# Kernel optimization log

Hardware: AMD Instinct MI355X
Metric: run time of the kernel (lower is better)

The kernel has to match this reference:

```python
import jax, jax.numpy as jnp
import numpy as np

H, W = 8, 64
HK, WK = 7, 11
N = H * W            # 512 tokens
C = 512              # embed_dim
HEADS = 8
HD = C // HEADS      # 64
SCALE = HD ** -0.5
B = 32


def build_local_mask():
    # Faithful port of the build() mask construction.
    m = np.ones([N, H + HK - 1, W + WK - 1], dtype=np.int32)
    for h in range(H):
        for w in range(W):
            m[h * W + w, h:h + HK, w:w + WK] = 0
    m = m[:, HK // 2:H + HK // 2, WK // 2:W + WK // 2].reshape(-1, N).astype(bool)
    mask = np.where(m, -1e30, 0.0).astype(np.float32)
    return jnp.asarray(mask.reshape(1, 1, N, N))


def setup_inputs() -> dict:
    key = jax.random.key(0)
    k1, k2, k3, k4 = jax.random.split(key, 4)
    return {
        "x": jax.random.normal(k1, (B, N, C), dtype=jnp.float32),
        "w_qkv": jax.random.normal(k2, (C, 3 * C), dtype=jnp.float32) * (C ** -0.5),
        "w_proj": jax.random.normal(k3, (C, C), dtype=jnp.float32) * (C ** -0.5),
        "b_proj": jax.random.normal(k4, (C,), dtype=jnp.float32) * 0.01,
        "mask": build_local_mask(),
    }


def reference(x, w_qkv, w_proj, b_proj, mask):
    b = x.shape[0]
    qkv = x @ w_qkv                                   # [B, N, 3C]
    qkv = qkv.reshape(b, N, 3, HEADS, HD)
    qkv = jnp.transpose(qkv, (2, 0, 3, 1, 4))          # [3, B, heads, N, hd]
    q, k, v = qkv[0], qkv[1], qkv[2]
    attn = jnp.einsum("bhnd,bhmd->bhnm", q * SCALE, k) + mask  # [B, heads, N, N]
    attn = jax.nn.softmax(attn, axis=-1)
    out = jnp.einsum("bhnm,bhmd->bhnd", attn, v)       # [B, heads, N, hd]
    out = jnp.transpose(out, (0, 2, 1, 3)).reshape(b, N, C)
    return out @ w_proj + b_proj
```

## Files before the change

kernel.cpp:

```cpp
#include <hip/hip_runtime.h>
#include <hip/hip_bf16.h>

typedef __attribute__((ext_vector_type(8))) __bf16 bf16x8;
typedef __attribute__((ext_vector_type(4))) float f32x4;

__device__ __forceinline__ unsigned short f2bf(float f) {
    unsigned int u = __float_as_uint(f);
    unsigned int r = u + 0x7FFFu + ((u >> 16) & 1u);
    return (unsigned short)(r >> 16);
}

__device__ __forceinline__ void async_copy16(const unsigned short* g, unsigned short* l) {
    __builtin_amdgcn_global_load_lds(
        (__attribute__((address_space(1))) void*)(g),
        (__attribute__((address_space(3))) void*)(l), 16, 0, 0);
}

__global__ __launch_bounds__(256) void cvt_f32_bf16(const float4* __restrict__ in,
                                                    uint4* __restrict__ out, int n8) {
    int i = blockIdx.x * blockDim.x + threadIdx.x;
    if (i >= n8) return;
    float4 a = in[2 * i], b = in[2 * i + 1];
    union { unsigned short s[8]; uint4 v; } r;
    r.s[0] = f2bf(a.x); r.s[1] = f2bf(a.y); r.s[2] = f2bf(a.z); r.s[3] = f2bf(a.w);
    r.s[4] = f2bf(b.x); r.s[5] = f2bf(b.y); r.s[6] = f2bf(b.z); r.s[7] = f2bf(b.w);
    out[i] = r.v;
}

__global__ __launch_bounds__(256) void transpose_cvt(const float* __restrict__ in,
                                                     unsigned short* __restrict__ out,
                                                     int R, int C) {
    __shared__ float tile[32][33];
    int c0 = blockIdx.x * 32, r0 = blockIdx.y * 32;
    int tx = threadIdx.x, ty = threadIdx.y;
    #pragma unroll
    for (int i = 0; i < 32; i += 8)
        tile[ty + i][tx] = in[(size_t)(r0 + ty + i) * C + c0 + tx];
    __syncthreads();
    #pragma unroll
    for (int i = 0; i < 32; i += 8)
        out[(size_t)(c0 + ty + i) * R + r0 + tx] = f2bf(tile[tx][ty + i]);
}

__device__ __forceinline__ void gemm_core_128(const unsigned short* __restrict__ A,
                                              const unsigned short* __restrict__ Bt,
                                              int K, int m0, int n0, f32x4 acc[4][4]) {
    __shared__ unsigned short As[128 * 64];
    __shared__ unsigned short Bs[128 * 64];
    const int lane = threadIdx.x & 63;
    const int wv   = threadIdx.x >> 6;
    const int wm = (wv >> 1) * 64, wn = (wv & 1) * 64;
    const int l15 = lane & 15, l16 = lane >> 4;

    f32x4 zz = {0.f, 0.f, 0.f, 0.f};
    #pragma unroll
    for (int i = 0; i < 4; ++i)
        #pragma unroll
        for (int j = 0; j < 4; ++j) acc[i][j] = zz;

    for (int k0 = 0; k0 < K; k0 += 64) {
        if (k0) __syncthreads();
        #pragma unroll
        for (int c = 0; c < 4; ++c) {
            int flat16 = c * 256 + (int)threadIdx.x;
            int r  = flat16 >> 3;
            int kk = (flat16 & 7) * 8;
            async_copy16(A  + (size_t)(m0 + r) * K + k0 + kk, As + flat16 * 8);
            async_copy16(Bt + (size_t)(n0 + r) * K + k0 + kk, Bs + flat16 * 8);
        }
        __syncthreads();
        #pragma unroll
        for (int kk = 0; kk < 64; kk += 32) {
            bf16x8 a[4], b[4];
            #pragma unroll
            for (int i = 0; i < 4; ++i)
                a[i] = *(const bf16x8*)(const void*)(As + (wm + i * 16 + l15) * 64 + kk + l16 * 8);
            #pragma unroll
            for (int i = 0; i < 4; ++i)
                b[i] = *(const bf16x8*)(const void*)(Bs + (wn + i * 16 + l15) * 64 + kk + l16 * 8);
            #pragma unroll
            for (int i = 0; i < 4; ++i)
                #pragma unroll
                for (int j = 0; j < 4; ++j)
                    acc[i][j] = __builtin_amdgcn_mfma_f32_16x16x32_bf16(a[i], b[j], acc[i][j], 0, 0, 0);
        }
    }
}

__global__ __launch_bounds__(512, 2) void gemm_qkv_bm(const unsigned short* __restrict__ xb,
                                                      const unsigned short* __restrict__ wT,
                                                      unsigned short* __restrict__ Qb,
                                                      unsigned short* __restrict__ Kb,
                                                      unsigned short* __restrict__ Vb) {
    constexpr int K = 512;
    __shared__ unsigned short As[256 * 64];
    __shared__ unsigned short Bs[128 * 64];

    const int tid  = threadIdx.x;
    const int lane = tid & 63;
    const int wv   = tid >> 6;
    const int wr = wv >> 1, wc = wv & 1;
    const int l15 = lane & 15, l16 = lane >> 4;

    const int bid = blockIdx.x;
    const int xcd = bid & 7, idx = bid >> 3;
    const int mt  = xcd * 8 + idx / 12;
    const int nt  = idx % 12;
    const int m0 = mt * 256, n0 = nt * 128;

    f32x4 acc[4][4];
    f32x4 zz = {0.f, 0.f, 0.f, 0.f};
    #pragma unroll
    for (int i = 0; i < 4; ++i)
        #pragma unroll
        for (int j = 0; j < 4; ++j) acc[i][j] = zz;

    const int r_st  = tid >> 3;
    const int kk_st = (tid & 7) * 8;
    const unsigned short* Arow = xb + (size_t)(m0 + r_st) * K + kk_st;
    const unsigned short* Brow = wT + (size_t)(n0 + r_st) * K + kk_st;

    for (int k0 = 0; k0 < K; k0 += 64) {
        if (k0) __syncthreads();
        #pragma unroll
        for (int c = 0; c < 4; ++c) {
            int flat16 = c * 512 + tid;
            async_copy16(Arow + (size_t)c * 64 * K + k0, As + flat16 * 8);
        }
        #pragma unroll
        for (int c = 0; c < 2; ++c) {
            int flat16 = c * 512 + tid;
            async_copy16(Brow + (size_t)c * 64 * K + k0, Bs + flat16 * 8);
        }
        __syncthreads();
        #pragma unroll
        for (int kk = 0; kk < 64; kk += 32) {
            bf16x8 a[4], b[4];
            #pragma unroll
            for (int i = 0; i < 4; ++i)
                a[i] = *(const bf16x8*)(const void*)(As + (wr * 64 + i * 16 + l15) * 64 + kk + l16 * 8);
            #pragma unroll
            for (int j = 0; j < 4; ++j)
                b[j] = *(const bf16x8*)(const void*)(Bs + (wc * 64 + j * 16 + l15) * 64 + kk + l16 * 8);
            #pragma unroll
            for (int i = 0; i < 4; ++i)
                #pragma unroll
                for (int j = 0; j < 4; ++j)
                    acc[i][j] = __builtin_amdgcn_mfma_f32_16x16x32_bf16(a[i], b[j], acc[i][j], 0, 0, 0);
        }
    }

    #pragma unroll
    for (int j = 0; j < 4; ++j) {
        int col = n0 + wc * 64 + j * 16 + l15;
        int t = col >> 9;
        int within = col & 511;
        int h = within >> 6, d = within & 63;
        unsigned short* dst = (t == 0) ? Qb : (t == 1) ? Kb : Vb;
        float scl = (t == 0) ? 0.125f : 1.0f;
        #pragma unroll
        for (int i = 0; i < 4; ++i)
            #pragma unroll
            for (int e = 0; e < 4; ++e) {
                int row = m0 + wr * 64 + i * 16 + (l16 << 2) + e;
                int bb = row >> 9, n = row & 511;
                dst[(((size_t)bb * 8 + h) * 512 + n) * 64 + d] = f2bf(acc[i][j][e] * scl);
            }
    }
}

__global__ __launch_bounds__(256, 4) void attn_kernel(const unsigned short* __restrict__ Qb,
                                                      const unsigned short* __restrict__ Kb,
                                                      const unsigned short* __restrict__ Vb,
                                                      unsigned short* __restrict__ Ob) {
    __shared__ unsigned short Ks[64 * 72];
    __shared__ unsigned short Vt[64 * 72];
    __shared__ unsigned short Ps[4 * 32 * 72];

    const int bh = blockIdx.x >> 2;
    const int qt = blockIdx.x & 3;
    const int tid = threadIdx.x;
    const int lane = tid & 63;
    const int wv = tid >> 6;
    const int l15 = lane & 15, l16 = lane >> 4;
    const int b = bh >> 3, h = bh & 7;

    const unsigned short* Qp = Qb + (size_t)bh * 512 * 64;
    const unsigned short* Kp = Kb + (size_t)bh * 512 * 64;
    const unsigned short* Vp = Vb + (size_t)bh * 512 * 64;
    unsigned short* Pw = Ps + wv * 32 * 72;

    const int qrow0 = qt * 128 + wv * 32;
    const int qh = qrow0 >> 6;
    const int wq0 = qrow0 & 63;
    const int dead_g = wq0 ? 0 : 3;

    unsigned int wbits = 0;
    {
        int qw[2] = { wq0 + l15, wq0 + 16 + l15 };
        #pragma unroll
        for (int qf = 0; qf < 2; ++qf)
            #pragma unroll
            for (int g = 0; g < 4; ++g)
                #pragma unroll
                for (int j = 0; j < 4; ++j) {
                    int kw = g * 16 + (l16 << 2) + j;
                    int dw = qw[qf] - kw; dw = dw < 0 ? -dw : dw;
                    wbits |= (dw <= 5 ? 1u : 0u) << (qf * 16 + g * 4 + j);
                }
    }

    bf16x8 bQ[2][2];
    #pragma unroll
    for (int qf = 0; qf < 2; ++qf)
        #pragma unroll
        for (int kf = 0; kf < 2; ++kf)
            bQ[qf][kf] = *(const bf16x8*)(const void*)(Qp + (size_t)(qrow0 + qf * 16 + l15) * 64 + kf * 32 + l16 * 8);

    f32x4 o[2][4];
    f32x4 zz = {0.f, 0.f, 0.f, 0.f};
    float mrow[2] = {-INFINITY, -INFINITY}, lrow[2] = {0.f, 0.f};
    #pragma unroll
    for (int qf = 0; qf < 2; ++qf)
        #pragma unroll
        for (int df = 0; df < 4; ++df) o[qf][df] = zz;

    for (int kh = 0; kh < 8; ++kh) {
        int dlo = kh - 2 * qt;
        if (dlo < -3 || dlo > 4) continue;
        __syncthreads();
        #pragma unroll
        for (int c = 0; c < 2; ++c) {
            int flat16 = c * 256 + tid;
            int key = flat16 >> 3, dk = (flat16 & 7) * 8;
            *(uint4*)(void*)(Ks + key * 72 + dk) = *(const uint4*)(const void*)(Kp + ((size_t)(kh * 64 + key) * 64 + dk));
        }
        #pragma unroll
        for (int c = 0; c < 2; ++c) {
            int flat16 = c * 256 + tid;
            int key = flat16 & 63, d8 = flat16 >> 6;
            union { uint4 v; unsigned short s[8]; } t;
            t.v = *(const uint4*)(const void*)(Vp + ((size_t)(kh * 64 + key) * 64 + d8 * 8));
            #pragma unroll
            for (int e = 0; e < 8; ++e) Vt[(d8 * 8 + e) * 72 + key] = t.s[e];
        }
        __syncthreads();

        int adq = qh - kh; adq = adq < 0 ? -adq : adq;
        if (adq > 3) continue;

        f32x4 s[2][4];
        #pragma unroll
        for (int qf = 0; qf < 2; ++qf)
            #pragma unroll
            for (int g = 0; g < 4; ++g) s[qf][g] = zz;
        #pragma unroll
        for (int g = 0; g < 4; ++g) {
            if (g == dead_g) continue;
            bf16x8 aK0 = *(const bf16x8*)(const void*)(Ks + (g * 16 + l15) * 72 + 0  + l16 * 8);
            bf16x8 aK1 = *(const bf16x8*)(const void*)(Ks + (g * 16 + l15) * 72 + 32 + l16 * 8);
            #pragma unroll
            for (int qf = 0; qf < 2; ++qf) {
                s[qf][g] = __builtin_amdgcn_mfma_f32_16x16x32_bf16(aK0, bQ[qf][0], s[qf][g], 0, 0, 0);
                s[qf][g] = __builtin_amdgcn_mfma_f32_16x16x32_bf16(aK1, bQ[qf][1], s[qf][g], 0, 0, 0);
            }
        }

        float tmax[2] = {-1e30f, -1e30f};
        #pragma unroll
        for (int qf = 0; qf < 2; ++qf) {
            #pragma unroll
            for (int g = 0; g < 4; ++g) {
                if (g == dead_g) continue;
                #pragma unroll
                for (int j = 0; j < 4; ++j) {
                    float v = ((wbits >> (qf * 16 + g * 4 + j)) & 1u) ? s[qf][g][j] : -1e30f;
                    s[qf][g][j] = v;
                    tmax[qf] = fmaxf(tmax[qf], v);
                }
            }
            float t = tmax[qf];
            t = fmaxf(t, __shfl_xor(t, 16));
            t = fmaxf(t, __shfl_xor(t, 32));
            tmax[qf] = t;
        }

        #pragma unroll
        for (int qf = 0; qf < 2; ++qf) {
            float mnew = fmaxf(mrow[qf], tmax[qf]);
            float fs = __expf(mrow[qf] - mnew);
            mrow[qf] = mnew;
            lrow[qf] *= fs;
            #pragma unroll
            for (int j = 0; j < 4; ++j) {
                float fso = __shfl(fs, (l16 << 2) + j);
                #pragma unroll
                for (int df = 0; df < 4; ++df) o[qf][df][j] *= fso;
            }
        }

        #pragma unroll
        for (int qf = 0; qf < 2; ++qf) {
            float lsum = 0.f;
            #pragma unroll
            for (int g = 0; g < 4; ++g) {
                unsigned int lo, hi;
                if (g == dead_g) {
                    lo = 0u; hi = 0u;
                } else {
                    float e0 = __expf(s[qf][g][0] - mrow[qf]);
                    float e1 = __expf(s[qf][g][1] - mrow[qf]);
                    float e2 = __expf(s[qf][g][2] - mrow[qf]);
                    float e3 = __expf(s[qf][g][3] - mrow[qf]);
                    lsum += (e0 + e1) + (e2 + e3);
                    asm("v_cvt_pk_bf16_f32 %0, %1, %2" : "=v"(lo) : "v"(e0), "v"(e1));
                    asm("v_cvt_pk_bf16_f32 %0, %1, %2" : "=v"(hi) : "v"(e2), "v"(e3));
                }
                uint2 w; w.x = lo; w.y = hi;
                *(uint2*)(void*)(Pw + (qf * 16 + l15) * 72 + g * 16 + (l16 << 2)) = w;
            }
            float t = lsum;
            t += __shfl_xor(t, 16);
            t += __shfl_xor(t, 32);
            lrow[qf] += t;
        }
        asm volatile("" ::: "memory");

        #pragma unroll
        for (int kf = 0; kf < 2; ++kf) {
            bf16x8 aP0 = *(const bf16x8*)(const void*)(Pw + (0 * 16 + l15) * 72 + kf * 32 + l16 * 8);
            bf16x8 aP1 = *(const bf16x8*)(const void*)(Pw + (1 * 16 + l15) * 72 + kf * 32 + l16 * 8);
            #pragma unroll
            for (int df = 0; df < 4; ++df) {
                bf16x8 bV = *(const bf16x8*)(const void*)(Vt + (df * 16 + l15) * 72 + kf * 32 + l16 * 8);
                o[0][df] = __builtin_amdgcn_mfma_f32_16x16x32_bf16(aP0, bV, o[0][df], 0, 0, 0);
                o[1][df] = __builtin_amdgcn_mfma_f32_16x16x32_bf16(aP1, bV, o[1][df], 0, 0, 0);
            }
        }
    }

    #pragma unroll
    for (int qf = 0; qf < 2; ++qf) {
        float linv = 1.0f / lrow[qf];
        #pragma unroll
        for (int j = 0; j < 4; ++j) {
            float lj = __shfl(linv, (l16 << 2) + j);
            int q = qrow0 + qf * 16 + (l16 << 2) + j;
            size_t base = ((size_t)b * 512 + q) * 512 + h * 64;
            #pragma unroll
            for (int df = 0; df < 4; ++df)
                Ob[base + df * 16 + l15] = f2bf(o[qf][df][j] * lj);
        }
    }
}

__global__ __launch_bounds__(256) void gemm_proj(const unsigned short* __restrict__ Ab,
                                                 const unsigned short* __restrict__ wT,
                                                 const float* __restrict__ bias,
                                                 float* __restrict__ out) {
    f32x4 acc[4][4];
    int m0 = blockIdx.y * 128, n0 = blockIdx.x * 128;
    gemm_core_128(Ab, wT, 512, m0, n0, acc);
    const int lane = threadIdx.x & 63, wv = threadIdx.x >> 6;
    const int wm = (wv >> 1) * 64, wn = (wv & 1) * 64;
    const int l15 = lane & 15, l16 = lane >> 4;
    #pragma unroll
    for (int j = 0; j < 4; ++j) {
        int col = n0 + wn + j * 16 + l15;
        float bb = bias[col];
        #pragma unroll
        for (int i = 0; i < 4; ++i)
            #pragma unroll
            for (int e = 0; e < 4; ++e) {
                int row = m0 + wm + i * 16 + (l16 << 2) + e;
                out[(size_t)row * 512 + col] = acc[i][j][e] + bb;
            }
    }
}

extern "C" void kernel_launch(void* const* d_in, const int* in_sizes, int n_in,
                              void* d_out, int out_size, void* d_ws, size_t ws_size,
                              hipStream_t stream) {
    const float* x      = (const float*)d_in[0];
    const float* w_qkv  = (const float*)d_in[1];
    const float* w_proj = (const float*)d_in[2];
    const float* b_proj = (const float*)d_in[3];
    float* out = (float*)d_out;

    char* ws = (char*)d_ws;
    unsigned short* xb     = (unsigned short*)(ws);
    unsigned short* wqkvT  = (unsigned short*)(ws + 16777216);
    unsigned short* wprojT = (unsigned short*)(ws + 18350080);
    unsigned short* Qb     = (unsigned short*)(ws + 18874368);
    unsigned short* Kb     = (unsigned short*)(ws + 35651584);
    unsigned short* Vb     = (unsigned short*)(ws + 52428800);
    unsigned short* Ob     = xb;

    cvt_f32_bf16<<<4096, 256, 0, stream>>>((const float4*)x, (uint4*)xb, 1048576);
    transpose_cvt<<<dim3(48, 16), dim3(32, 8), 0, stream>>>(w_qkv, wqkvT, 512, 1536);
    transpose_cvt<<<dim3(16, 16), dim3(32, 8), 0, stream>>>(w_proj, wprojT, 512, 512);
    gemm_qkv_bm<<<768, 512, 0, stream>>>(xb, wqkvT, Qb, Kb, Vb);
    attn_kernel<<<1024, 256, 0, stream>>>(Qb, Kb, Vb, Ob);
    gemm_proj<<<dim3(4, 128), 256, 0, stream>>>(Ob, wprojT, b_proj, out);
}
```

Measured before the change: 120.5 us.

## Fuse x fp32-to-bf16 conversion into QKV GEMM A-tile loads

Removes the separate cvt_f32_bf16 pass over x and has the QKV GEMM stage fp32 x tiles into LDS, converting them to bf16 at fragment-load time with packed cvt instructions. This drops one full read and write of x through memory and one kernel launch. In exchange the A tile uses twice the LDS bytes and the block tiling drops from 256x128 with 512 threads and XCD-aware ordering to 128x128 with 256 threads on a plain 2D grid. It also adds conversion ALU work inside the GEMM inner loop and re-reads fp32 x once per N tile.

```diff
diff --git a/kernel.cpp b/kernel.cpp
--- a/kernel.cpp
+++ b/kernel.cpp
@@ -16,15 +16,21 @@
         (__attribute__((address_space(3))) void*)(l), 16, 0, 0);
 }
 
-__global__ __launch_bounds__(256) void cvt_f32_bf16(const float4* __restrict__ in,
-                                                    uint4* __restrict__ out, int n8) {
-    int i = blockIdx.x * blockDim.x + threadIdx.x;
-    if (i >= n8) return;
-    float4 a = in[2 * i], b = in[2 * i + 1];
-    union { unsigned short s[8]; uint4 v; } r;
-    r.s[0] = f2bf(a.x); r.s[1] = f2bf(a.y); r.s[2] = f2bf(a.z); r.s[3] = f2bf(a.w);
-    r.s[4] = f2bf(b.x); r.s[5] = f2bf(b.y); r.s[6] = f2bf(b.z); r.s[7] = f2bf(b.w);
-    out[i] = r.v;
+__device__ __forceinline__ void async_copy16f(const float* g, float* l) {
+    __builtin_amdgcn_global_load_lds(
+        (__attribute__((address_space(1))) void*)(g),
+        (__attribute__((address_space(3))) void*)(l), 16, 0, 0);
+}
+
+__device__ __forceinline__ bf16x8 cvt8(const float* p) {
+    f32x4 lo = *(const f32x4*)(const void*)p;
+    f32x4 hi = *(const f32x4*)(const void*)(p + 4);
+    union { unsigned int u[4]; bf16x8 v; } r;
+    asm("v_cvt_pk_bf16_f32 %0, %1, %2" : "=v"(r.u[0]) : "v"(lo[0]), "v"(lo[1]));
+    asm("v_cvt_pk_bf16_f32 %0, %1, %2" : "=v"(r.u[1]) : "v"(lo[2]), "v"(lo[3]));
+    asm("v_cvt_pk_bf16_f32 %0, %1, %2" : "=v"(r.u[2]) : "v"(hi[0]), "v"(hi[1]));
+    asm("v_cvt_pk_bf16_f32 %0, %1, %2" : "=v"(r.u[3]) : "v"(hi[2]), "v"(hi[3]));
+    return r.v;
 }
 
 __global__ __launch_bounds__(256) void transpose_cvt(const float* __restrict__ in,
@@ -87,26 +93,21 @@
     }
 }
 
-__global__ __launch_bounds__(512, 2) void gemm_qkv_bm(const unsigned short* __restrict__ xb,
-                                                      const unsigned short* __restrict__ wT,
-                                                      unsigned short* __restrict__ Qb,
-                                                      unsigned short* __restrict__ Kb,
-                                                      unsigned short* __restrict__ Vb) {
+__global__ __launch_bounds__(256) void gemm_qkv_f32a(const float* __restrict__ x,
+                                                     const unsigned short* __restrict__ wT,
+                                                     unsigned short* __restrict__ Qb,
+                                                     unsigned short* __restrict__ Kb,
+                                                     unsigned short* __restrict__ Vb) {
     constexpr int K = 512;
-    __shared__ unsigned short As[256 * 64];
-    __shared__ unsigned short Bs[128 * 64];
+    __shared__ float          Asf[128 * 64];
+    __shared__ unsigned short Bs [128 * 64];
 
     const int tid  = threadIdx.x;
     const int lane = tid & 63;
     const int wv   = tid >> 6;
-    const int wr = wv >> 1, wc = wv & 1;
+    const int wm = (wv >> 1) * 64, wn = (wv & 1) * 64;
     const int l15 = lane & 15, l16 = lane >> 4;
-
-    const int bid = blockIdx.x;
-    const int xcd = bid & 7, idx = bid >> 3;
-    const int mt  = xcd * 8 + idx / 12;
-    const int nt  = idx % 12;
-    const int m0 = mt * 256, n0 = nt * 128;
+    const int m0 = blockIdx.y * 128, n0 = blockIdx.x * 128;
 
     f32x4 acc[4][4];
     f32x4 zz = {0.f, 0.f, 0.f, 0.f};
@@ -115,22 +116,21 @@
         #pragma unroll
         for (int j = 0; j < 4; ++j) acc[i][j] = zz;
 
-    const int r_st  = tid >> 3;
-    const int kk_st = (tid & 7) * 8;
-    const unsigned short* Arow = xb + (size_t)(m0 + r_st) * K + kk_st;
-    const unsigned short* Brow = wT + (size_t)(n0 + r_st) * K + kk_st;
-
     for (int k0 = 0; k0 < K; k0 += 64) {
         if (k0) __syncthreads();
         #pragma unroll
+        for (int c = 0; c < 8; ++c) {
+            int flat16 = c * 256 + tid;
+            int r  = flat16 >> 4;
+            int k4 = (flat16 & 15) * 4;
+            async_copy16f(x + (size_t)(m0 + r) * K + k0 + k4, Asf + flat16 * 4);
+        }
+        #pragma unroll
         for (int c = 0; c < 4; ++c) {
-            int flat16 = c * 512 + tid;
-            async_copy16(Arow + (size_t)c * 64 * K + k0, As + flat16 * 8);
-        }
-        #pragma unroll
-        for (int c = 0; c < 2; ++c) {
-            int flat16 = c * 512 + tid;
-            async_copy16(Brow + (size_t)c * 64 * K + k0, Bs + flat16 * 8);
+            int flat16 = c * 256 + tid;
+            int r   = flat16 >> 3;
+            int kk8 = (flat16 & 7) * 8;
+            async_copy16(wT + (size_t)(n0 + r) * K + k0 + kk8, Bs + flat16 * 8);
         }
         __syncthreads();
         #pragma unroll
@@ -138,10 +138,10 @@
             bf16x8 a[4], b[4];
             #pragma unroll
             for (int i = 0; i < 4; ++i)
-                a[i] = *(const bf16x8*)(const void*)(As + (wr * 64 + i * 16 + l15) * 64 + kk + l16 * 8);
+                a[i] = cvt8(Asf + (wm + i * 16 + l15) * 64 + kk + l16 * 8);
             #pragma unroll
             for (int j = 0; j < 4; ++j)
-                b[j] = *(const bf16x8*)(const void*)(Bs + (wc * 64 + j * 16 + l15) * 64 + kk + l16 * 8);
+                b[j] = *(const bf16x8*)(const void*)(Bs + (wn + j * 16 + l15) * 64 + kk + l16 * 8);
             #pragma unroll
             for (int i = 0; i < 4; ++i)
                 #pragma unroll
@@ -152,7 +152,7 @@
 
     #pragma unroll
     for (int j = 0; j < 4; ++j) {
-        int col = n0 + wc * 64 + j * 16 + l15;
+        int col = n0 + wn + j * 16 + l15;
         int t = col >> 9;
         int within = col & 511;
         int h = within >> 6, d = within & 63;
@@ -162,9 +162,9 @@
         for (int i = 0; i < 4; ++i)
             #pragma unroll
             for (int e = 0; e < 4; ++e) {
-                int row = m0 + wr * 64 + i * 16 + (l16 << 2) + e;
-                int bb = row >> 9, n = row & 511;
-                dst[(((size_t)bb * 8 + h) * 512 + n) * 64 + d] = f2bf(acc[i][j][e] * scl);
+                int row = m0 + wm + i * 16 + (l16 << 2) + e;
+                int b = row >> 9, n = row & 511;
+                dst[(((size_t)b * 8 + h) * 512 + n) * 64 + d] = f2bf(acc[i][j][e] * scl);
             }
     }
 }
@@ -388,18 +388,16 @@
     float* out = (float*)d_out;
 
     char* ws = (char*)d_ws;
-    unsigned short* xb     = (unsigned short*)(ws);
+    unsigned short* Ob     = (unsigned short*)(ws);
     unsigned short* wqkvT  = (unsigned short*)(ws + 16777216);
     unsigned short* wprojT = (unsigned short*)(ws + 18350080);
     unsigned short* Qb     = (unsigned short*)(ws + 18874368);
     unsigned short* Kb     = (unsigned short*)(ws + 35651584);
     unsigned short* Vb     = (unsigned short*)(ws + 52428800);
-    unsigned short* Ob     = xb;
-
-    cvt_f32_bf16<<<4096, 256, 0, stream>>>((const float4*)x, (uint4*)xb, 1048576);
+
     transpose_cvt<<<dim3(48, 16), dim3(32, 8), 0, stream>>>(w_qkv, wqkvT, 512, 1536);
     transpose_cvt<<<dim3(16, 16), dim3(32, 8), 0, stream>>>(w_proj, wprojT, 512, 512);
-    gemm_qkv_bm<<<768, 512, 0, stream>>>(xb, wqkvT, Qb, Kb, Vb);
+    gemm_qkv_f32a<<<dim3(12, 128), 256, 0, stream>>>(x, wqkvT, Qb, Kb, Vb);
     attn_kernel<<<1024, 256, 0, stream>>>(Qb, Kb, Vb, Ob);
     gemm_proj<<<dim3(4, 128), 256, 0, stream>>>(Ob, wprojT, b_proj, out);
 }
```

Measured after the change: 128.1 us. 6.3% more time.
